# Kernel optimization log

Measured on AMD Instinct MI355X. Metric: run time of the kernel, lower is better.

Reference implementation:

```python
import jax, jax.numpy as jnp
import numpy as np

N_NODES = 100000
N_EDGES = 3200000
BATCH = 16
LAYER_NUMBER = 4


def setup_inputs() -> dict:
    key = jax.random.key(0)
    k1, k2, k3, k4 = jax.random.split(key, 4)
    x = jax.random.normal(k1, (N_NODES, BATCH), dtype=jnp.float32)
    # learnable per-edge weights (log1p(counts) at init in the original; the
    # parameter itself is what is learned, so a plain random init is faithful)
    weights = jax.random.normal(k2, (N_EDGES,), dtype=jnp.float32)
    row = jax.random.randint(k3, (N_EDGES,), 0, N_NODES, dtype=jnp.int64)
    col = jax.random.randint(k4, (N_EDGES,), 0, N_NODES, dtype=jnp.int64)
    return {"x": x, "weights": weights, "row": row, "col": col}


def reference(x, weights, row, col):
    # Repeated sparse COO SpMM: y <- A @ y, applied layer_number times,
    # where A[row[e], col[e]] = weights[e].
    def step(y, _):
        msg = weights[:, None] * y[col]                      # [E, B] gather + scale
        y_new = jax.ops.segment_sum(msg, row, num_segments=N_NODES)  # [N, B] scatter-add
        return y_new, None

    y, _ = jax.lax.scan(step, x, None, length=LAYER_NUMBER)
    return y
```

## Files before the change

kernel.cpp:

```cpp
#include <hip/hip_runtime.h>

#define N_NODES 100000
#define N_EDGES 3200000
#define BATCH 16
#define BKT_SHIFT 6
#define BKT_NODES 64
#define K_BUCKETS 1563
#define NB 512
#define SUB (N_EDGES / NB)
#define FT 512
#define SCAN_T 256
#define SCAN_C 7
#define CAP 4096

__global__ void hist_kernel(const int* __restrict__ row, int* __restrict__ blk_cnt) {
    __shared__ int lh[K_BUCKETS];
    int t = threadIdx.x, blk = blockIdx.x;
    for (int k = t; k < K_BUCKETS; k += 256) lh[k] = 0;
    __syncthreads();
    int base = blk * SUB;
    for (int e = base + t; e < base + SUB; e += 256)
        atomicAdd(&lh[row[e] >> BKT_SHIFT], 1);
    __syncthreads();
    for (int k = t; k < K_BUCKETS; k += 256)
        blk_cnt[k * NB + blk] = lh[k];
}

__global__ void colscan_kernel(int* __restrict__ blk_cnt, int* __restrict__ totals) {
    int wid = (blockIdx.x * blockDim.x + threadIdx.x) >> 6;
    int lane = threadIdx.x & 63;
    if (wid >= K_BUCKETS) return;
    int* p = &blk_cnt[wid * NB + lane * 8];
    int4 a = ((int4*)p)[0];
    int4 b = ((int4*)p)[1];
    int lt = a.x + a.y + a.z + a.w + b.x + b.y + b.z + b.w;
    int pref = lt;
    #pragma unroll
    for (int off = 1; off < 64; off <<= 1) {
        int v = __shfl_up(pref, off, 64);
        if (lane >= off) pref += v;
    }
    int run = pref - lt;
    int4 oa, ob;
    oa.x = run; run += a.x;
    oa.y = run; run += a.y;
    oa.z = run; run += a.z;
    oa.w = run; run += a.w;
    ob.x = run; run += b.x;
    ob.y = run; run += b.y;
    ob.z = run; run += b.z;
    ob.w = run; run += b.w;
    ((int4*)p)[0] = oa;
    ((int4*)p)[1] = ob;
    int tot = __shfl(pref, 63, 64);
    if (lane == 0) totals[wid] = tot;
}

__global__ void scan_kernel(const int* __restrict__ totals, int* __restrict__ bptr,
                            int* __restrict__ row_ptr) {
    __shared__ int s[SCAN_T];
    int t = threadIdx.x;
    int loc[SCAN_C];
    int sum = 0;
    for (int i = 0; i < SCAN_C; i++) {
        int idx = t * SCAN_C + i;
        int v = (idx < K_BUCKETS) ? totals[idx] : 0;
        loc[i] = v;
        sum += v;
    }
    s[t] = sum;
    __syncthreads();
    for (int off = 1; off < SCAN_T; off <<= 1) {
        int x = (t >= off) ? s[t - off] : 0;
        __syncthreads();
        s[t] += x;
        __syncthreads();
    }
    int excl = s[t] - sum;
    for (int i = 0; i < SCAN_C; i++) {
        int idx = t * SCAN_C + i;
        if (idx < K_BUCKETS) bptr[idx] = excl;
        excl += loc[i];
    }
    if (t == 0) { bptr[K_BUCKETS] = N_EDGES; row_ptr[N_NODES] = N_EDGES; }
}

__global__ void __launch_bounds__(FT) fill_kernel(
        const int* __restrict__ row, const int* __restrict__ col,
        const float* __restrict__ w,
        const int* __restrict__ bptr, const int* __restrict__ blk_cnt,
        uint2* __restrict__ entries) {
    __shared__ uint2 sbuf[SUB];
    __shared__ int lbeg[K_BUCKETS];
    __shared__ int lcur[K_BUCKETS];
    __shared__ int sscan[FT];
    int t = threadIdx.x, blk = blockIdx.x;
    for (int k = t; k < K_BUCKETS; k += FT) lcur[k] = 0;
    __syncthreads();
    int base = blk * SUB;
    for (int e = base + t; e < base + SUB; e += FT)
        atomicAdd(&lcur[row[e] >> BKT_SHIFT], 1);
    __syncthreads();
    int loc[4];
    int sum = 0;
    #pragma unroll
    for (int j = 0; j < 4; j++) {
        int k = t * 4 + j;
        int v = (k < K_BUCKETS) ? lcur[k] : 0;
        loc[j] = v;
        sum += v;
    }
    sscan[t] = sum;
    __syncthreads();
    for (int off = 1; off < FT; off <<= 1) {
        int x = (t >= off) ? sscan[t - off] : 0;
        __syncthreads();
        sscan[t] += x;
        __syncthreads();
    }
    int excl = sscan[t] - sum;
    #pragma unroll
    for (int j = 0; j < 4; j++) {
        int k = t * 4 + j;
        if (k < K_BUCKETS) { lbeg[k] = excl; lcur[k] = excl; }
        excl += loc[j];
    }
    __syncthreads();
    for (int e = base + t; e < base + SUB; e += FT) {
        int r = row[e];
        int bkt = r >> BKT_SHIFT;
        int pos = atomicAdd(&lcur[bkt], 1);
        sbuf[pos] = make_uint2(((unsigned)(r & (BKT_NODES - 1)) << 17) | (unsigned)col[e],
                               __float_as_uint(w[e]));
    }
    __syncthreads();
    int lane = t & 3;
    for (int k = (t >> 2); k < K_BUCKETS; k += FT / 4) {
        int lb = lbeg[k];
        int le = lcur[k];
        int dst = bptr[k] + blk_cnt[k * NB + blk];
        for (int i = lb + lane; i < le; i += 4)
            entries[dst + (i - lb)] = sbuf[i];
    }
}

__global__ void nodesort_kernel(const int* __restrict__ bptr, uint2* __restrict__ entries,
                                int* __restrict__ row_ptr) {
    __shared__ uint2 ebuf[CAP];
    __shared__ int nh[BKT_NODES];
    __shared__ int nc[BKT_NODES];
    int t = threadIdx.x, b = blockIdx.x;
    int beg = bptr[b], end = bptr[b + 1];
    int n = min(end - beg, CAP);
    if (t < BKT_NODES) nh[t] = 0;
    __syncthreads();
    for (int k = t; k < n; k += 256) {
        uint2 r = entries[beg + k];
        ebuf[k] = r;
        atomicAdd(&nh[r.x >> 17], 1);
    }
    __syncthreads();
    if (t == 0) {
        int acc = 0;
        for (int i = 0; i < BKT_NODES; i++) {
            int v = nh[i];
            int node = b * BKT_NODES + i;
            if (node < N_NODES) row_ptr[node] = beg + acc;
            nc[i] = acc;
            acc += v;
        }
    }
    __syncthreads();
    for (int k = t; k < n; k += 256) {
        uint2 r = ebuf[k];
        int pos = atomicAdd(&nc[r.x >> 17], 1);
        entries[beg + pos] = r;
    }
}

__global__ void __launch_bounds__(256) pull_kernel(const float* __restrict__ y,
                            const uint2* __restrict__ entries,
                            const int* __restrict__ row_ptr,
                            float* __restrict__ out) {
    int tid = blockIdx.x * blockDim.x + threadIdx.x;
    int node = tid >> 2;
    int q = tid & 3;
    if (node >= N_NODES) return;
    int beg = row_ptr[node];
    int end = row_ptr[node + 1];
    float4 acc = make_float4(0.f, 0.f, 0.f, 0.f);
    if (beg < end) {
        int lim = end - 1;
        uint2 r[8];
        #pragma unroll
        for (int j = 0; j < 8; j++) r[j] = entries[min(beg + j, lim)];
        int i = beg;
        while (i + 8 <= end) {
            float4 yv[8];
            #pragma unroll
            for (int j = 0; j < 8; j++)
                yv[j] = *(const float4*)&y[(r[j].x & 0x1FFFFu) * BATCH + q * 4];
            uint2 nx[8];
            #pragma unroll
            for (int j = 0; j < 8; j++)
                nx[j] = entries[min(i + 8 + j, lim)];
            #pragma unroll
            for (int j = 0; j < 8; j++) {
                float wj = __uint_as_float(r[j].y);
                acc.x += wj * yv[j].x;
                acc.y += wj * yv[j].y;
                acc.z += wj * yv[j].z;
                acc.w += wj * yv[j].w;
            }
            #pragma unroll
            for (int j = 0; j < 8; j++) r[j] = nx[j];
            i += 8;
        }
        if (i < end) {
            float4 yv[8];
            #pragma unroll
            for (int j = 0; j < 8; j++)
                yv[j] = *(const float4*)&y[(r[j].x & 0x1FFFFu) * BATCH + q * 4];
            #pragma unroll
            for (int j = 0; j < 8; j++)
                if (i + j < end) {
                    float wj = __uint_as_float(r[j].y);
                    acc.x += wj * yv[j].x;
                    acc.y += wj * yv[j].y;
                    acc.z += wj * yv[j].z;
                    acc.w += wj * yv[j].w;
                }
        }
    }
    *(float4*)&out[node * BATCH + q * 4] = acc;
}

extern "C" void kernel_launch(void* const* d_in, const int* in_sizes, int n_in,
                              void* d_out, int out_size, void* d_ws, size_t ws_size,
                              hipStream_t stream) {
    const float* x   = (const float*)d_in[0];
    const float* w   = (const float*)d_in[1];
    const int*   row = (const int*)d_in[2];
    const int*   col = (const int*)d_in[3];
    float*       out = (float*)d_out;

    char* p = (char*)d_ws;
    uint2* entries = (uint2*)p;  p += (size_t)N_EDGES * sizeof(uint2);
    float* buf     = (float*)p;
    int*   blk_cnt = (int*)buf;
    p += (size_t)N_NODES * BATCH * sizeof(float);
    int* totals  = (int*)p;      p += 8192;
    int* bptr    = (int*)p;      p += 8192;
    int* row_ptr = (int*)p;

    hist_kernel<<<NB, 256, 0, stream>>>(row, blk_cnt);
    colscan_kernel<<<(K_BUCKETS * 64 + 255) / 256, 256, 0, stream>>>(blk_cnt, totals);
    scan_kernel<<<1, SCAN_T, 0, stream>>>(totals, bptr, row_ptr);
    fill_kernel<<<NB, FT, 0, stream>>>(row, col, w, bptr, blk_cnt, entries);
    nodesort_kernel<<<K_BUCKETS, 256, 0, stream>>>(bptr, entries, row_ptr);

    const int pgrid = (N_NODES * 4 + 255) / 256;
    pull_kernel<<<pgrid, 256, 0, stream>>>(x,   entries, row_ptr, buf);
    pull_kernel<<<pgrid, 256, 0, stream>>>(buf, entries, row_ptr, out);
    pull_kernel<<<pgrid, 256, 0, stream>>>(out, entries, row_ptr, buf);
    pull_kernel<<<pgrid, 256, 0, stream>>>(buf, entries, row_ptr, out);
}
```

Measured before the change: 329.6 us.

## Split batch into two 8-wide planes so each SpMM pass gathers a smaller vector

After: 571.9 us. 1.74x slower.

```diff
diff --git a/kernel.cpp b/kernel.cpp
--- a/kernel.cpp
+++ b/kernel.cpp
@@ -12,6 +12,8 @@
 #define SCAN_T 256
 #define SCAN_C 7
 #define CAP 4096
+
+typedef float v4f __attribute__((ext_vector_type(4)));
 
 __global__ void hist_kernel(const int* __restrict__ row, int* __restrict__ blk_cnt) {
     __shared__ int lh[K_BUCKETS];
@@ -178,32 +180,51 @@
     }
 }
 
-__global__ void __launch_bounds__(256) pull_kernel(const float* __restrict__ y,
-                            const uint2* __restrict__ entries,
-                            const int* __restrict__ row_ptr,
-                            float* __restrict__ out) {
+__global__ void split_kernel(const float* __restrict__ x, float* __restrict__ planes) {
+    int node = blockIdx.x * blockDim.x + threadIdx.x;
+    if (node >= N_NODES) return;
+    const float4* src = (const float4*)&x[node * BATCH];
+    float4 a0 = src[0], a1 = src[1], a2 = src[2], a3 = src[3];
+    float4* p0 = (float4*)&planes[(size_t)node * 8];
+    p0[0] = a0; p0[1] = a1;
+    float4* p1 = (float4*)&planes[(size_t)N_NODES * 8 + (size_t)node * 8];
+    p1[0] = a2; p1[1] = a3;
+}
+
+__device__ __forceinline__ uint2 nt_load_e(const uint2* p) {
+    unsigned long long v = __builtin_nontemporal_load((const unsigned long long*)p);
+    return make_uint2((unsigned)v, (unsigned)(v >> 32));
+}
+
+__global__ void __launch_bounds__(256) pull_half_kernel(
+        const float* __restrict__ yplanes,
+        const uint2* __restrict__ entries,
+        const int* __restrict__ row_ptr,
+        float* __restrict__ out,
+        int half, int out_interleaved) {
     int tid = blockIdx.x * blockDim.x + threadIdx.x;
-    int node = tid >> 2;
-    int q = tid & 3;
+    int node = tid >> 1;
+    int q = tid & 1;
     if (node >= N_NODES) return;
-    int beg = row_ptr[node];
-    int end = row_ptr[node + 1];
+    const float* in = yplanes + (size_t)half * N_NODES * 8 + q * 4;
+    int beg = __builtin_nontemporal_load(&row_ptr[node]);
+    int end = __builtin_nontemporal_load(&row_ptr[node + 1]);
     float4 acc = make_float4(0.f, 0.f, 0.f, 0.f);
     if (beg < end) {
         int lim = end - 1;
         uint2 r[8];
         #pragma unroll
-        for (int j = 0; j < 8; j++) r[j] = entries[min(beg + j, lim)];
+        for (int j = 0; j < 8; j++) r[j] = nt_load_e(&entries[min(beg + j, lim)]);
         int i = beg;
         while (i + 8 <= end) {
             float4 yv[8];
             #pragma unroll
             for (int j = 0; j < 8; j++)
-                yv[j] = *(const float4*)&y[(r[j].x & 0x1FFFFu) * BATCH + q * 4];
+                yv[j] = *(const float4*)&in[(r[j].x & 0x1FFFFu) * 8];
             uint2 nx[8];
             #pragma unroll
             for (int j = 0; j < 8; j++)
-                nx[j] = entries[min(i + 8 + j, lim)];
+                nx[j] = nt_load_e(&entries[min(i + 8 + j, lim)]);
             #pragma unroll
             for (int j = 0; j < 8; j++) {
                 float wj = __uint_as_float(r[j].y);
@@ -220,7 +241,7 @@
             float4 yv[8];
             #pragma unroll
             for (int j = 0; j < 8; j++)
-                yv[j] = *(const float4*)&y[(r[j].x & 0x1FFFFu) * BATCH + q * 4];
+                yv[j] = *(const float4*)&in[(r[j].x & 0x1FFFFu) * 8];
             #pragma unroll
             for (int j = 0; j < 8; j++)
                 if (i + j < end) {
@@ -232,7 +253,11 @@
                 }
         }
     }
-    *(float4*)&out[node * BATCH + q * 4] = acc;
+    size_t dst = out_interleaved
+        ? (size_t)node * BATCH + half * 8 + q * 4
+        : (size_t)half * N_NODES * 8 + (size_t)node * 8 + q * 4;
+    v4f av = {acc.x, acc.y, acc.z, acc.w};
+    __builtin_nontemporal_store(av, (v4f*)&out[dst]);
 }
 
 extern "C" void kernel_launch(void* const* d_in, const int* in_sizes, int n_in,
@@ -259,9 +284,15 @@
     fill_kernel<<<NB, FT, 0, stream>>>(row, col, w, bptr, blk_cnt, entries);
     nodesort_kernel<<<K_BUCKETS, 256, 0, stream>>>(bptr, entries, row_ptr);
 
-    const int pgrid = (N_NODES * 4 + 255) / 256;
-    pull_kernel<<<pgrid, 256, 0, stream>>>(x,   entries, row_ptr, buf);
-    pull_kernel<<<pgrid, 256, 0, stream>>>(buf, entries, row_ptr, out);
-    pull_kernel<<<pgrid, 256, 0, stream>>>(out, entries, row_ptr, buf);
-    pull_kernel<<<pgrid, 256, 0, stream>>>(buf, entries, row_ptr, out);
-}
+    split_kernel<<<(N_NODES + 255) / 256, 256, 0, stream>>>(x, out);
+
+    const int pgrid = (N_NODES * 2 + 255) / 256;
+    pull_half_kernel<<<pgrid, 256, 0, stream>>>(out, entries, row_ptr, buf, 0, 0);
+    pull_half_kernel<<<pgrid, 256, 0, stream>>>(out, entries, row_ptr, buf, 1, 0);
+    pull_half_kernel<<<pgrid, 256, 0, stream>>>(buf, entries, row_ptr, out, 0, 0);
+    pull_half_kernel<<<pgrid, 256, 0, stream>>>(buf, entries, row_ptr, out, 1, 0);
+    pull_half_kernel<<<pgrid, 256, 0, stream>>>(out, entries, row_ptr, buf, 0, 0);
+    pull_half_kernel<<<pgrid, 256, 0, stream>>>(out, entries, row_ptr, buf, 1, 0);
+    pull_half_kernel<<<pgrid, 256, 0, stream>>>(buf, entries, row_ptr, out, 0, 1);
+    pull_half_kernel<<<pgrid, 256, 0, stream>>>(buf, entries, row_ptr, out, 1, 1);
+}
```

## Fuse per-bucket node sort with first SpMM layer from shared memory

Applied to the files above, without the earlier changes.

Measured after the change: 316.2 us. 1.04x faster.

```diff
diff --git a/kernel.cpp b/kernel.cpp
--- a/kernel.cpp
+++ b/kernel.cpp
@@ -144,38 +144,97 @@
     }
 }
 
-__global__ void nodesort_kernel(const int* __restrict__ bptr, uint2* __restrict__ entries,
-                                int* __restrict__ row_ptr) {
+__global__ void __launch_bounds__(256) nodesort_pull1_kernel(
+        const int* __restrict__ bptr, uint2* __restrict__ entries,
+        int* __restrict__ row_ptr,
+        const float* __restrict__ x, float* __restrict__ out) {
     __shared__ uint2 ebuf[CAP];
     __shared__ int nh[BKT_NODES];
     __shared__ int nc[BKT_NODES];
+    __shared__ int nstart[BKT_NODES + 1];
     int t = threadIdx.x, b = blockIdx.x;
     int beg = bptr[b], end = bptr[b + 1];
     int n = min(end - beg, CAP);
     if (t < BKT_NODES) nh[t] = 0;
     __syncthreads();
-    for (int k = t; k < n; k += 256) {
-        uint2 r = entries[beg + k];
-        ebuf[k] = r;
-        atomicAdd(&nh[r.x >> 17], 1);
-    }
-    __syncthreads();
-    if (t == 0) {
-        int acc = 0;
-        for (int i = 0; i < BKT_NODES; i++) {
-            int v = nh[i];
-            int node = b * BKT_NODES + i;
-            if (node < N_NODES) row_ptr[node] = beg + acc;
-            nc[i] = acc;
-            acc += v;
-        }
-    }
-    __syncthreads();
-    for (int k = t; k < n; k += 256) {
-        uint2 r = ebuf[k];
-        int pos = atomicAdd(&nc[r.x >> 17], 1);
-        entries[beg + pos] = r;
-    }
+    uint2 rs[16];
+    int cnt = 0;
+    #pragma unroll
+    for (int i = 0; i < 16; i++) {
+        int k = t + i * 256;
+        if (k < n) {
+            uint2 r = entries[beg + k];
+            rs[i] = r;
+            atomicAdd(&nh[r.x >> 17], 1);
+            cnt = i + 1;
+        }
+    }
+    __syncthreads();
+    if (t < BKT_NODES) {
+        int v = nh[t];
+        int pref = v;
+        #pragma unroll
+        for (int off = 1; off < BKT_NODES; off <<= 1) {
+            int u = __shfl_up(pref, off, 64);
+            if (t >= off) pref += u;
+        }
+        int excl = pref - v;
+        nstart[t] = excl;
+        nc[t] = excl;
+        if (t == BKT_NODES - 1) nstart[BKT_NODES] = pref;
+        int node = b * BKT_NODES + t;
+        if (node < N_NODES) row_ptr[node] = beg + excl;
+    }
+    __syncthreads();
+    #pragma unroll
+    for (int i = 0; i < 16; i++) {
+        if (i < cnt) {
+            uint2 r = rs[i];
+            int pos = atomicAdd(&nc[r.x >> 17], 1);
+            ebuf[pos] = r;
+            entries[beg + pos] = r;
+        }
+    }
+    __syncthreads();
+    int ln = t >> 2, q = t & 3;
+    int node = b * BKT_NODES + ln;
+    if (node >= N_NODES) return;
+    int s = nstart[ln], e = nstart[ln + 1];
+    float4 acc = make_float4(0.f, 0.f, 0.f, 0.f);
+    int i = s;
+    while (i + 8 <= e) {
+        uint2 r0 = ebuf[i + 0], r1 = ebuf[i + 1], r2 = ebuf[i + 2], r3 = ebuf[i + 3];
+        uint2 r4 = ebuf[i + 4], r5 = ebuf[i + 5], r6 = ebuf[i + 6], r7 = ebuf[i + 7];
+        float4 y0 = *(const float4*)&x[(r0.x & 0x1FFFFu) * BATCH + q * 4];
+        float4 y1 = *(const float4*)&x[(r1.x & 0x1FFFFu) * BATCH + q * 4];
+        float4 y2 = *(const float4*)&x[(r2.x & 0x1FFFFu) * BATCH + q * 4];
+        float4 y3 = *(const float4*)&x[(r3.x & 0x1FFFFu) * BATCH + q * 4];
+        float4 y4 = *(const float4*)&x[(r4.x & 0x1FFFFu) * BATCH + q * 4];
+        float4 y5 = *(const float4*)&x[(r5.x & 0x1FFFFu) * BATCH + q * 4];
+        float4 y6 = *(const float4*)&x[(r6.x & 0x1FFFFu) * BATCH + q * 4];
+        float4 y7 = *(const float4*)&x[(r7.x & 0x1FFFFu) * BATCH + q * 4];
+        float w0 = __uint_as_float(r0.y), w1 = __uint_as_float(r1.y);
+        float w2 = __uint_as_float(r2.y), w3 = __uint_as_float(r3.y);
+        float w4 = __uint_as_float(r4.y), w5 = __uint_as_float(r5.y);
+        float w6 = __uint_as_float(r6.y), w7 = __uint_as_float(r7.y);
+        acc.x += w0 * y0.x; acc.y += w0 * y0.y; acc.z += w0 * y0.z; acc.w += w0 * y0.w;
+        acc.x += w1 * y1.x; acc.y += w1 * y1.y; acc.z += w1 * y1.z; acc.w += w1 * y1.w;
+        acc.x += w2 * y2.x; acc.y += w2 * y2.y; acc.z += w2 * y2.z; acc.w += w2 * y2.w;
+        acc.x += w3 * y3.x; acc.y += w3 * y3.y; acc.z += w3 * y3.z; acc.w += w3 * y3.w;
+        acc.x += w4 * y4.x; acc.y += w4 * y4.y; acc.z += w4 * y4.z; acc.w += w4 * y4.w;
+        acc.x += w5 * y5.x; acc.y += w5 * y5.y; acc.z += w5 * y5.z; acc.w += w5 * y5.w;
+        acc.x += w6 * y6.x; acc.y += w6 * y6.y; acc.z += w6 * y6.z; acc.w += w6 * y6.w;
+        acc.x += w7 * y7.x; acc.y += w7 * y7.y; acc.z += w7 * y7.z; acc.w += w7 * y7.w;
+        i += 8;
+    }
+    for (; i < e; i++) {
+        uint2 r = ebuf[i];
+        float4 yv = *(const float4*)&x[(r.x & 0x1FFFFu) * BATCH + q * 4];
+        float wj = __uint_as_float(r.y);
+        acc.x += wj * yv.x; acc.y += wj * yv.y;
+        acc.z += wj * yv.z; acc.w += wj * yv.w;
+    }
+    *(float4*)&out[node * BATCH + q * 4] = acc;
 }
 
 __global__ void __launch_bounds__(256) pull_kernel(const float* __restrict__ y,
@@ -257,10 +316,9 @@
     colscan_kernel<<<(K_BUCKETS * 64 + 255) / 256, 256, 0, stream>>>(blk_cnt, totals);
     scan_kernel<<<1, SCAN_T, 0, stream>>>(totals, bptr, row_ptr);
     fill_kernel<<<NB, FT, 0, stream>>>(row, col, w, bptr, blk_cnt, entries);
-    nodesort_kernel<<<K_BUCKETS, 256, 0, stream>>>(bptr, entries, row_ptr);
-
+
+    nodesort_pull1_kernel<<<K_BUCKETS, 256, 0, stream>>>(bptr, entries, row_ptr, x, buf);
     const int pgrid = (N_NODES * 4 + 255) / 256;
-    pull_kernel<<<pgrid, 256, 0, stream>>>(x,   entries, row_ptr, buf);
     pull_kernel<<<pgrid, 256, 0, stream>>>(buf, entries, row_ptr, out);
     pull_kernel<<<pgrid, 256, 0, stream>>>(out, entries, row_ptr, buf);
     pull_kernel<<<pgrid, 256, 0, stream>>>(buf, entries, row_ptr, out);
```
